# Performance work log

Hardware: AMD Instinct MI355X
Metric: run time of the kernel (lower is better)

## Reference

```python
import jax, jax.numpy as jnp
import numpy as np

EMBED = 1024
HEADS = 16
HDIM = 64
FF = 4 * EMBED
EPS = 1e-5


def layer_norm(x, g, b):
    mu = jnp.mean(x, axis=-1, keepdims=True)
    var = jnp.var(x, axis=-1, keepdims=True)
    return (x - mu) * jax.lax.rsqrt(var + EPS) * g + b


def setup_inputs() -> dict:
    key = jax.random.key(0)
    ks = jax.random.split(key, 12)
    s = lambda fan_in: 1.0 / np.sqrt(fan_in)
    return {
        "x": jax.random.normal(ks[0], (2, 2048, EMBED), jnp.float32),
        "w_qkv": jax.random.uniform(ks[1], (EMBED, 3 * HEADS * HDIM), jnp.float32, -s(EMBED), s(EMBED)),
        "w_proj": jax.random.uniform(ks[2], (HEADS * HDIM, EMBED), jnp.float32, -s(HEADS * HDIM), s(HEADS * HDIM)),
        "b_proj": jax.random.uniform(ks[3], (EMBED,), jnp.float32, -s(HEADS * HDIM), s(HEADS * HDIM)),
        "w1": jax.random.uniform(ks[4], (EMBED, FF), jnp.float32, -s(EMBED), s(EMBED)),
        "b1": jax.random.uniform(ks[5], (FF,), jnp.float32, -s(EMBED), s(EMBED)),
        "w2": jax.random.uniform(ks[6], (FF, EMBED), jnp.float32, -s(FF), s(FF)),
        "b2": jax.random.uniform(ks[7], (EMBED,), jnp.float32, -s(FF), s(FF)),
        "g1": jnp.ones((EMBED,), jnp.float32),
        "be1": jnp.zeros((EMBED,), jnp.float32),
        "g2": jnp.ones((EMBED,), jnp.float32),
        "be2": jnp.zeros((EMBED,), jnp.float32),
    }


def reference(x, w_qkv, w_proj, b_proj, w1, b1, w2, b2, g1, be1, g2, be2):
    bs, seq, _ = x.shape
    # --- MHA on pre-norm ---
    h = layer_norm(x, g1, be1)
    qkv = h @ w_qkv  # [b, s, 3*H*D]
    qkv = qkv.reshape(bs, seq, HEADS, 3, HDIM)
    q = qkv[:, :, :, 0, :]  # [b, s, h, d]
    k = qkv[:, :, :, 1, :]
    v = qkv[:, :, :, 2, :]
    attn = jnp.einsum("bqhd,bkhd->bhqk", q, k) / np.sqrt(HDIM)
    causal = jnp.tril(jnp.ones((seq, seq), bool))
    attn = jnp.where(causal, attn, -jnp.inf)
    attn = jax.nn.softmax(attn, axis=-1)
    out = jnp.einsum("bhqk,bkhd->bhqd", attn, v)
    # Faithful to original bug: .view without transposing heads back.
    out = out.reshape(bs, seq, HEADS * HDIM)
    out = out @ w_proj + b_proj
    x = x + out
    # --- FFN on pre-norm ---
    h2 = layer_norm(x, g2, be2)
    ff = jax.nn.relu(h2 @ w1 + b1) @ w2 + b2
    return x + ff
```

## Files before the change

### kernel.cpp

```cpp
#include <hip/hip_runtime.h>
#include <cstdint>

#define EMBED 1024
#define HEADS 16
#define HDIM  64
#define SEQ   2048
#define BATCH 2
#define ROWS  (BATCH*SEQ)

typedef __bf16 bf16x8 __attribute__((ext_vector_type(8)));
typedef float  f32x4  __attribute__((ext_vector_type(4)));
typedef float  f32x16 __attribute__((ext_vector_type(16)));
typedef unsigned int uint32x2 __attribute__((ext_vector_type(2)));

__device__ __forceinline__ unsigned short f2bf(float f) {
    union { float f; uint32_t u; } v; v.f = f;
    uint32_t r = v.u + 0x7fffu + ((v.u >> 16) & 1u);
    return (unsigned short)(r >> 16);
}

__device__ __forceinline__ uint32_t cvtpk_bf16(float lo, float hi) {
    uint32_t r;
    asm("v_cvt_pk_bf16_f32 %0, %1, %2" : "=v"(r) : "v"(lo), "v"(hi));
    return r;
}

__device__ __forceinline__ float fexp2(float x) {
    float r;
    asm("v_exp_f32 %0, %1" : "=v"(r) : "v"(x));
    return r;
}

#define GLDS(src, dst) __builtin_amdgcn_global_load_lds( \
    (const __attribute__((address_space(1))) uint32_t*)(src), \
    (__attribute__((address_space(3))) uint32_t*)(dst), 16, 0, 0)

__global__ __launch_bounds__(256) void k_transpose_all(
    const float* __restrict__ w_qkv, const float* __restrict__ w_proj,
    const float* __restrict__ w1,    const float* __restrict__ w2,
    unsigned short* __restrict__ wqkvT, unsigned short* __restrict__ wprojT,
    unsigned short* __restrict__ w1T,   unsigned short* __restrict__ w2T)
{
    int b = blockIdx.x;
    const float* in; unsigned short* out; int N, K, nx;
    if (b < 3072)      {           in = w_qkv;  out = wqkvT;  K = 1024; N = 3072; nx = 96; }
    else if (b < 4096) { b -= 3072; in = w_proj; out = wprojT; K = 1024; N = 1024; nx = 32; }
    else if (b < 8192) { b -= 4096; in = w1;     out = w1T;    K = 1024; N = 4096; nx = 128; }
    else               { b -= 8192; in = w2;     out = w2T;    K = 4096; N = 1024; nx = 32; }
    const int n0 = (b % nx) * 32, k0 = (b / nx) * 32;

    __shared__ float tile[32][33];
    const int tx = threadIdx.x & 31, ty = threadIdx.x >> 5;
#pragma unroll
    for (int r = 0; r < 4; ++r)
        tile[ty + 8*r][tx] = in[(size_t)(k0 + ty + 8*r) * N + n0 + tx];
    __syncthreads();
#pragma unroll
    for (int r = 0; r < 4; ++r)
        out[(size_t)(n0 + ty + 8*r) * K + k0 + tx] = f2bf(tile[tx][ty + 8*r]);
}

__global__ __launch_bounds__(256) void k_layernorm(
    const float* __restrict__ x, const float* __restrict__ g, const float* __restrict__ b,
    unsigned short* __restrict__ h)
{
    const int row = blockIdx.x, t = threadIdx.x;
    float4 v = ((const float4*)(x + (size_t)row * EMBED))[t];
    float s = v.x + v.y + v.z + v.w;
    float q = v.x*v.x + v.y*v.y + v.z*v.z + v.w*v.w;
#pragma unroll
    for (int off = 32; off >= 1; off >>= 1) {
        s += __shfl_xor(s, off, 64);
        q += __shfl_xor(q, off, 64);
    }
    __shared__ float ss[4], sq[4];
    if ((t & 63) == 0) { ss[t >> 6] = s; sq[t >> 6] = q; }
    __syncthreads();
    s = ss[0] + ss[1] + ss[2] + ss[3];
    q = sq[0] + sq[1] + sq[2] + sq[3];
    const float mu  = s * (1.0f / EMBED);
    const float var = q * (1.0f / EMBED) - mu * mu;
    const float rs  = rsqrtf(var + 1e-5f);
    float4 gv = ((const float4*)g)[t];
    float4 bv = ((const float4*)b)[t];
    ushort4 o;
    o.x = f2bf((v.x - mu) * rs * gv.x + bv.x);
    o.y = f2bf((v.y - mu) * rs * gv.y + bv.y);
    o.z = f2bf((v.z - mu) * rs * gv.z + bv.z);
    o.w = f2bf((v.w - mu) * rs * gv.w + bv.w);
    ((ushort4*)(h + (size_t)row * EMBED))[t] = o;
}

template<int FLAGS, typename OutT>
__global__ __launch_bounds__(512) void k_gemm_bt(
    const unsigned short* __restrict__ A,
    const unsigned short* __restrict__ BT,
    const float* __restrict__ bias,
    const float* __restrict__ resid,
    OutT* __restrict__ C,
    int M, int N, int K)
{
    __shared__ uint4 ldsv[8192];
    char* base = (char*)ldsv;
    char* aL = base;
    char* bL = base + 16384;
    const int t = threadIdx.x, l = t & 63, w = t >> 6;
    const int pos = w & 3, kh = w >> 2;
    const int qr = pos >> 1, qc = pos & 1;
    const int g = l >> 4, c = l & 15;

    const int gx = gridDim.x;
    const int lin = blockIdx.y * gx + blockIdx.x;
    const int cpx = (gx * gridDim.y) >> 3;
    const int swz = (lin & 7) * cpx + (lin >> 3);
    const int row0 = (swz / gx) * 128, col0 = (swz % gx) * 128;

    const int swc = (((l & 7) ^ (l >> 3)) * 8);
    const int rA0 = w*16 + (l >> 3), rA1 = rA0 + 8;
    const unsigned short* aS0 = A  + (size_t)(row0 + rA0) * K + swc;
    const unsigned short* aS1 = A  + (size_t)(row0 + rA1) * K + swc;
    const unsigned short* bS0 = BT + (size_t)(col0 + rA0) * K + swc;
    const unsigned short* bS1 = BT + (size_t)(col0 + rA1) * K + swc;
    const int dst0 = w * 2048, dst1 = w * 2048 + 1024;

    f32x4 acc[4][4];
#pragma unroll
    for (int m = 0; m < 4; ++m)
#pragma unroll
        for (int n = 0; n < 4; ++n) acc[m][n] = f32x4{0.f, 0.f, 0.f, 0.f};

    auto stage = [&](int kt, int bo) {
        const size_t ko = (size_t)kt * 64;
        GLDS(aS0 + ko, aL + bo + dst0);
        GLDS(aS1 + ko, aL + bo + dst1);
        GLDS(bS0 + ko, bL + bo + dst0);
        GLDS(bS1 + ko, bL + bo + dst1);
    };
    auto compute = [&](int bo) {
        const int chb = ((kh*4 + g) ^ (c & 7)) * 16;
        bf16x8 af[4], bfr[4];
#pragma unroll
        for (int m = 0; m < 4; ++m)
            af[m] = *(const bf16x8*)(aL + bo + (qr*64 + m*16 + c) * 128 + chb);
#pragma unroll
        for (int n = 0; n < 4; ++n)
            bfr[n] = *(const bf16x8*)(bL + bo + (qc*64 + n*16 + c) * 128 + chb);
        __builtin_amdgcn_s_setprio(1);
#pragma unroll
        for (int m = 0; m < 4; ++m)
#pragma unroll
            for (int n = 0; n < 4; ++n)
                acc[m][n] = __builtin_amdgcn_mfma_f32_16x16x32_bf16(af[m], bfr[n], acc[m][n], 0, 0, 0);
        __builtin_amdgcn_s_setprio(0);
    };

    const int nkt = K >> 6;
    stage(0, 0);
    stage(1, 32768);
    for (int kt = 0; kt < nkt; ++kt) {
        const int bo = (kt & 3) * 32768;
        if (kt + 2 < nkt) {
            stage(kt + 2, ((kt + 2) & 3) * 32768);
            asm volatile("s_waitcnt vmcnt(8)" ::: "memory");
        } else if (kt + 1 < nkt) {
            asm volatile("s_waitcnt vmcnt(4)" ::: "memory");
        } else {
            asm volatile("s_waitcnt vmcnt(0)" ::: "memory");
        }
        __builtin_amdgcn_s_barrier();
        compute(bo);
    }

    asm volatile("s_waitcnt lgkmcnt(0)" ::: "memory");
    __builtin_amdgcn_s_barrier();
    if (kh) {
#pragma unroll
        for (int m = 0; m < 4; ++m)
#pragma unroll
            for (int n = 0; n < 4; ++n)
                *(f32x4*)(base + (((pos*16 + m*4 + n) * 64) + l) * 16) = acc[m][n];
    }
    asm volatile("s_waitcnt lgkmcnt(0)" ::: "memory");
    __builtin_amdgcn_s_barrier();

    if (!kh) {
#pragma unroll
        for (int m = 0; m < 4; ++m) {
            const int rb = row0 + qr*64 + m*16 + g*4;
#pragma unroll
            for (int n = 0; n < 4; ++n) {
                const f32x4 part = *(const f32x4*)(base + (((pos*16 + m*4 + n) * 64) + l) * 16);
                const int col = col0 + qc*64 + n*16 + c;
                float bv = 0.f;
                if constexpr ((FLAGS & 1) != 0) bv = bias[col];
#pragma unroll
                for (int j = 0; j < 4; ++j) {
                    float v = acc[m][n][j] + part[j] + bv;
                    if constexpr ((FLAGS & 2) != 0) v = fmaxf(v, 0.f);
                    if constexpr ((FLAGS & 4) != 0) v += resid[(size_t)(rb + j) * N + col];
                    if constexpr (sizeof(OutT) == 2) C[(size_t)(rb + j) * N + col] = (OutT)f2bf(v);
                    else                             C[(size_t)(rb + j) * N + col] = v;
                }
            }
        }
    }
}

template<int FLAGS, typename OutT>
__global__ __launch_bounds__(512) __attribute__((amdgpu_waves_per_eu(2, 2)))
void k_gemm256(
    const unsigned short* __restrict__ A,
    const unsigned short* __restrict__ BT,
    const float* __restrict__ bias,
    OutT* __restrict__ C,
    unsigned short* __restrict__ Qo,
    unsigned short* __restrict__ Ko,
    unsigned short* __restrict__ Vo,
    int M, int N, int K)
{
    __shared__ uint4 ldsv[8192];
    char* base = (char*)ldsv;
    const int t = threadIdx.x, l = t & 63, w = t >> 6;
    const int wr = w >> 2, wc = w & 3;
    const int g = l >> 4, c = l & 15;

    const int gx = gridDim.x;
    const int lin = blockIdx.y * gx + blockIdx.x;
    const int cpx = (gx * gridDim.y) >> 3;
    const int swz = (lin & 7) * cpx + (lin >> 3);
    const int row0 = (swz / gx) * 256, col0 = (swz % gx) * 256;

    const int srow = l >> 2;
    const int sch  = (l & 3) ^ ((l >> 3) & 3);
    const unsigned short* aS0 = A  + (size_t)(row0 + w*32 +      srow) * K + sch*8;
    const unsigned short* aS1 = A  + (size_t)(row0 + w*32 + 16 + srow) * K + sch*8;
    const unsigned short* bS0 = BT + (size_t)(col0 + w*32 +      srow) * K + sch*8;
    const unsigned short* bS1 = BT + (size_t)(col0 + w*32 + 16 + srow) * K + sch*8;
    const int dA0 = w*2048, dA1 = w*2048 + 1024;

    f32x4 acc[8][4];
#pragma unroll
    for (int m = 0; m < 8; ++m)
#pragma unroll
        for (int n = 0; n < 4; ++n) acc[m][n] = f32x4{0.f, 0.f, 0.f, 0.f};

    auto stage = [&](int kt, int bo) {
        const size_t ko = (size_t)kt * 32;
        GLDS(aS0 + ko, base + bo + dA0);
        GLDS(aS1 + ko, base + bo + dA1);
        GLDS(bS0 + ko, base + bo + 16384 + dA0);
        GLDS(bS1 + ko, base + bo + 16384 + dA1);
    };
    auto compute = [&](int bo) {
        const int chb = (g ^ ((c >> 1) & 3)) * 16;
        bf16x8 af[8], bfr[4];
#pragma unroll
        for (int m = 0; m < 8; ++m)
            af[m] = *(const bf16x8*)(base + bo + (wr*128 + m*16 + c) * 64 + chb);
#pragma unroll
        for (int n = 0; n < 4; ++n)
            bfr[n] = *(const bf16x8*)(base + bo + 16384 + (wc*64 + n*16 + c) * 64 + chb);
        __builtin_amdgcn_s_setprio(1);
#pragma unroll
        for (int m = 0; m < 8; ++m)
#pragma unroll
            for (int n = 0; n < 4; ++n)
                acc[m][n] = __builtin_amdgcn_mfma_f32_16x16x32_bf16(af[m], bfr[n], acc[m][n], 0, 0, 0);
        __builtin_amdgcn_s_setprio(0);
    };

    const int nkt = K >> 5;
    stage(0, 0);
    stage(1, 32768);
    for (int kt = 0; kt < nkt; ++kt) {
        const int bo = (kt & 3) * 32768;
        if (kt + 2 < nkt) {
            stage(kt + 2, ((kt + 2) & 3) * 32768);
            asm volatile("s_waitcnt vmcnt(8)" ::: "memory");
        } else if (kt + 1 < nkt) {
            asm volatile("s_waitcnt vmcnt(4)" ::: "memory");
        } else {
            asm volatile("s_waitcnt vmcnt(0)" ::: "memory");
        }
        __builtin_amdgcn_s_barrier();
        compute(bo);
    }

    if constexpr ((FLAGS & 8) != 0) {
#pragma unroll
        for (int m = 0; m < 8; ++m) {
            const int rb = row0 + wr*128 + m*16 + g*4;
            const int b  = rb >> 11;
            const int q0 = rb & 2047;
#pragma unroll
            for (int n = 0; n < 4; ++n) {
                const int col = col0 + wc*64 + n*16 + c;
                const int hh  = col / 192;
                const int rem = col - hh * 192;
                const int tt  = rem >> 6;
                const int d   = rem & 63;
                const int bhh = b * HEADS + hh;
                if (tt == 2) {
                    const int st_e = q0 >> 6, kk = q0 & 63;
                    const int f_e  = (d >> 5) * 4 + (kk >> 4);
                    const int ln_e = ((kk >> 3) & 1) * 32 + (d & 31);
                    const int e0   = kk & 7;
                    ushort4 o;
                    o.x = f2bf(acc[m][n][0]); o.y = f2bf(acc[m][n][1]);
                    o.z = f2bf(acc[m][n][2]); o.w = f2bf(acc[m][n][3]);
                    *(ushort4*)(Vo + (size_t)bhh * (SEQ*HDIM) + st_e*4096 + f_e*512 + ln_e*8 + e0) = o;
                } else if (tt == 1) {
                    const int st_e = q0 >> 6;
                    const int f_e  = ((q0 >> 5) & 1) * 4 + (d >> 4);
                    const int lq_e = q0 & 31;
                    const int ln_b = ((d >> 3) & 1) * 32;
                    const int e_e  = d & 7;
                    unsigned short* dst = Ko + (size_t)bhh * (SEQ*HDIM) + st_e*4096 + f_e*512
                                             + (ln_b + lq_e)*8 + e_e;
#pragma unroll
                    for (int j = 0; j < 4; ++j)
                        dst[j*8] = f2bf(acc[m][n][j]);
                } else {
                    unsigned short* dst = Qo + ((size_t)bhh * SEQ + q0) * HDIM + d;
#pragma unroll
                    for (int j = 0; j < 4; ++j)
                        dst[(size_t)j * HDIM] = f2bf(acc[m][n][j]);
                }
            }
        }
    } else {
#pragma unroll
        for (int m = 0; m < 8; ++m) {
            const int rb = row0 + wr*128 + m*16 + g*4;
#pragma unroll
            for (int n = 0; n < 4; ++n) {
                const int col = col0 + wc*64 + n*16 + c;
                float bv = 0.f;
                if constexpr ((FLAGS & 1) != 0) bv = bias[col];
#pragma unroll
                for (int j = 0; j < 4; ++j) {
                    float v = acc[m][n][j] + bv;
                    if constexpr ((FLAGS & 2) != 0) v = fmaxf(v, 0.f);
                    if constexpr (sizeof(OutT) == 2) C[(size_t)(rb + j) * N + col] = (OutT)f2bf(v);
                    else                             C[(size_t)(rb + j) * N + col] = v;
                }
            }
        }
    }
}

__global__ __launch_bounds__(512) __attribute__((amdgpu_waves_per_eu(2, 2)))
void k_attention(
    const unsigned short* __restrict__ Qb,
    const unsigned short* __restrict__ Kf,
    const unsigned short* __restrict__ Vf,
    unsigned short* __restrict__ out)
{
    const int t = threadIdx.x, l = t & 63, w = t >> 6;
    const int lq = l & 31, hi = l >> 5;
    const int bid = blockIdx.x;
    const int sbid = (bid & 7) * 32 + (bid >> 3);
    const int bh = sbid >> 3, j = sbid & 7;
    const int qb = (w < 4) ? (4*j + w) : (63 - 4*j - (w - 4));
    const int q  = qb * 32 + lq;

    const unsigned short* Qh  = Qb + (size_t)bh * SEQ * HDIM;
    const unsigned short* Kfh = Kf + (size_t)bh * SEQ * HDIM + l*8;
    const unsigned short* Vfh = Vf + (size_t)bh * SEQ * HDIM + l*8;

    const bf16x8 qf0 = *(const bf16x8*)(Qh + (size_t)q * HDIM      + hi*8);
    const bf16x8 qf1 = *(const bf16x8*)(Qh + (size_t)q * HDIM + 16 + hi*8);
    const bf16x8 qf2 = *(const bf16x8*)(Qh + (size_t)q * HDIM + 32 + hi*8);
    const bf16x8 qf3 = *(const bf16x8*)(Qh + (size_t)q * HDIM + 48 + hi*8);

    f32x16 oT0, oT1;
#pragma unroll
    for (int i = 0; i < 16; ++i) { oT0[i] = 0.f; oT1[i] = 0.f; }
    float lacc0 = 0.f, lacc1 = 0.f, lacc2 = 0.f, lacc3 = 0.f;
    const float kSc = 0.18033688011112042f;
    const int nst = (qb >> 1) + 1;

    bf16x8 kA0, kA1, kA2, kA3, kA4, kA5, kA6, kA7;
    bf16x8 kB0, kB1, kB2, kB3, kB4, kB5, kB6, kB7;

#define LOADK(stv, KF) do {                                                     \
    const unsigned short* kp_ = Kfh + (size_t)(stv) * 4096;                     \
    KF##0 = *(const bf16x8*)(kp_ +    0); KF##1 = *(const bf16x8*)(kp_ +  512); \
    KF##2 = *(const bf16x8*)(kp_ + 1024); KF##3 = *(const bf16x8*)(kp_ + 1536); \
    KF##4 = *(const bf16x8*)(kp_ + 2048); KF##5 = *(const bf16x8*)(kp_ + 2560); \
    KF##6 = *(const bf16x8*)(kp_ + 3072); KF##7 = *(const bf16x8*)(kp_ + 3584); \
} while (0)

#define STEP(stv, KF) do {                                                      \
    const int kv0_ = (stv) * 64;                                                \
    const unsigned short* vp_ = Vfh + (size_t)(stv) * 4096;                     \
    bf16x8 vf0_ = *(const bf16x8*)(vp_ +    0), vf1_ = *(const bf16x8*)(vp_ +  512); \
    bf16x8 vf2_ = *(const bf16x8*)(vp_ + 1024), vf3_ = *(const bf16x8*)(vp_ + 1536); \
    bf16x8 vf4_ = *(const bf16x8*)(vp_ + 2048), vf5_ = *(const bf16x8*)(vp_ + 2560); \
    bf16x8 vf6_ = *(const bf16x8*)(vp_ + 3072), vf7_ = *(const bf16x8*)(vp_ + 3584); \
    f32x16 sA_, sB_;                                                            \
    _Pragma("unroll")                                                           \
    for (int i = 0; i < 16; ++i) { sA_[i] = 0.f; sB_[i] = 0.f; }               \
    __builtin_amdgcn_s_setprio(1);                                              \
    sA_ = __builtin_amdgcn_mfma_f32_32x32x16_bf16(KF##0, qf0, sA_, 0, 0, 0);    \
    sA_ = __builtin_amdgcn_mfma_f32_32x32x16_bf16(KF##1, qf1, sA_, 0, 0, 0);    \
    sA_ = __builtin_amdgcn_mfma_f32_32x32x16_bf16(KF##2, qf2, sA_, 0, 0, 0);    \
    sA_ = __builtin_amdgcn_mfma_f32_32x32x16_bf16(KF##3, qf3, sA_, 0, 0, 0);    \
    sB_ = __builtin_amdgcn_mfma_f32_32x32x16_bf16(KF##4, qf0, sB_, 0, 0, 0);    \
    sB_ = __builtin_amdgcn_mfma_f32_32x32x16_bf16(KF##5, qf1, sB_, 0, 0, 0);    \
    sB_ = __builtin_amdgcn_mfma_f32_32x32x16_bf16(KF##6, qf2, sB_, 0, 0, 0);    \
    sB_ = __builtin_amdgcn_mfma_f32_32x32x16_bf16(KF##7, qf3, sB_, 0, 0, 0);    \
    __builtin_amdgcn_s_setprio(0);                                              \
    float p_[32];                                                               \
    if ((stv) == nst - 1) {                                                     \
        _Pragma("unroll")                                                       \
        for (int r = 0; r < 16; ++r) {                                          \
            const int key_ = kv0_ + (r & 3) + 8*(r >> 2) + 4*hi;                \
            p_[r]      = (key_      <= q) ? fexp2(sA_[r] * kSc) : 0.f;          \
            p_[16 + r] = (key_ + 32 <= q) ? fexp2(sB_[r] * kSc) : 0.f;          \
        }                                                                       \
    } else {                                                                    \
        _Pragma("unroll")                                                       \
        for (int r = 0; r < 16; ++r) {                                          \
            p_[r]      = fexp2(sA_[r] * kSc);                                   \
            p_[16 + r] = fexp2(sB_[r] * kSc);                                   \
        }                                                                       \
    }                                                                           \
    _Pragma("unroll")                                                           \
    for (int i = 0; i < 32; i += 4) {                                           \
        lacc0 += p_[i]; lacc1 += p_[i+1]; lacc2 += p_[i+2]; lacc3 += p_[i+3];   \
    }                                                                           \
    bf16x8 pa_[4];                                                              \
    _Pragma("unroll")                                                           \
    for (int ks = 0; ks < 4; ++ks) {                                            \
        const int b8_ = ks * 8;                                                 \
        uint32x2 rA_ = __builtin_amdgcn_permlane32_swap(                        \
            cvtpk_bf16(p_[b8_+0], p_[b8_+1]), cvtpk_bf16(p_[b8_+4], p_[b8_+5]), false, false); \
        uint32x2 rB_ = __builtin_amdgcn_permlane32_swap(                        \
            cvtpk_bf16(p_[b8_+2], p_[b8_+3]), cvtpk_bf16(p_[b8_+6], p_[b8_+7]), false, false); \
        union { uint32_t u[4]; bf16x8 v; } pk_;                                 \
        pk_.u[0] = rA_[0]; pk_.u[1] = rB_[0]; pk_.u[2] = rA_[1]; pk_.u[3] = rB_[1]; \
        pa_[ks] = pk_.v;                                                        \
    }                                                                           \
    __builtin_amdgcn_s_setprio(1);                                              \
    oT0 = __builtin_amdgcn_mfma_f32_32x32x16_bf16(vf0_, pa_[0], oT0, 0, 0, 0);  \
    oT0 = __builtin_amdgcn_mfma_f32_32x32x16_bf16(vf1_, pa_[1], oT0, 0, 0, 0);  \
    oT0 = __builtin_amdgcn_mfma_f32_32x32x16_bf16(vf2_, pa_[2], oT0, 0, 0, 0);  \
    oT0 = __builtin_amdgcn_mfma_f32_32x32x16_bf16(vf3_, pa_[3], oT0, 0, 0, 0);  \
    oT1 = __builtin_amdgcn_mfma_f32_32x32x16_bf16(vf4_, pa_[0], oT1, 0, 0, 0);  \
    oT1 = __builtin_amdgcn_mfma_f32_32x32x16_bf16(vf5_, pa_[1], oT1, 0, 0, 0);  \
    oT1 = __builtin_amdgcn_mfma_f32_32x32x16_bf16(vf6_, pa_[2], oT1, 0, 0, 0);  \
    oT1 = __builtin_amdgcn_mfma_f32_32x32x16_bf16(vf7_, pa_[3], oT1, 0, 0, 0);  \
    __builtin_amdgcn_s_setprio(0);                                              \
} while (0)

    LOADK(0, kA);
    int st = 0;
    for (;;) {
        if (st + 1 < nst) LOADK(st + 1, kB);
        STEP(st, kA);
        if (++st >= nst) break;
        if (st + 1 < nst) LOADK(st + 1, kA);
        STEP(st, kB);
        if (++st >= nst) break;
    }
#undef LOADK
#undef STEP

    float lsum = (lacc0 + lacc1) + (lacc2 + lacc3);
    lsum += __shfl_xor(lsum, 32, 64);
    const float inv = 1.f / lsum;
    unsigned short* ob = out + ((size_t)bh * SEQ + q) * HDIM;
#pragma unroll
    for (int m2 = 0; m2 < 4; ++m2) {
        ushort4 o0, o1;
        o0.x = f2bf(oT0[m2*4+0] * inv); o0.y = f2bf(oT0[m2*4+1] * inv);
        o0.z = f2bf(oT0[m2*4+2] * inv); o0.w = f2bf(oT0[m2*4+3] * inv);
        o1.x = f2bf(oT1[m2*4+0] * inv); o1.y = f2bf(oT1[m2*4+1] * inv);
        o1.z = f2bf(oT1[m2*4+2] * inv); o1.w = f2bf(oT1[m2*4+3] * inv);
        *(ushort4*)(ob +      m2*8 + hi*4) = o0;
        *(ushort4*)(ob + 32 + m2*8 + hi*4) = o1;
    }
}

extern "C" void kernel_launch(void* const* d_in, const int* in_sizes, int n_in,
                              void* d_out, int out_size, void* d_ws, size_t ws_size,
                              hipStream_t stream)
{
    (void)in_sizes; (void)n_in; (void)out_size; (void)ws_size;
    const float* x      = (const float*)d_in[0];
    const float* w_qkv  = (const float*)d_in[1];
    const float* w_proj = (const float*)d_in[2];
    const float* b_proj = (const float*)d_in[3];
    const float* w1     = (const float*)d_in[4];
    const float* b1     = (const float*)d_in[5];
    const float* w2     = (const float*)d_in[6];
    const float* b2     = (const float*)d_in[7];
    const float* g1     = (const float*)d_in[8];
    const float* be1    = (const float*)d_in[9];
    const float* g2     = (const float*)d_in[10];
    const float* be2    = (const float*)d_in[11];

    char* ws = (char*)d_ws;
    size_t o = 0;
    auto take = [&](size_t bytes) -> char* {
        char* p = ws + o;
        o += (bytes + 255) & ~(size_t)255;
        return p;
    };
    unsigned short* wqkvT  = (unsigned short*)take(3072ull * 1024 * 2);
    unsigned short* wprojT = (unsigned short*)take(1024ull * 1024 * 2);
    unsigned short* w1T    = (unsigned short*)take(4096ull * 1024 * 2);
    unsigned short* w2T    = (unsigned short*)take(1024ull * 4096 * 2);
    unsigned short* h      = (unsigned short*)take(4096ull * 1024 * 2);
    unsigned short* Qb     = (unsigned short*)take(4096ull * 1024 * 2);
    unsigned short* Kfb    = (unsigned short*)take(4096ull * 1024 * 2);
    unsigned short* Vfb    = (unsigned short*)take(4096ull * 1024 * 2);
    unsigned short* attno  = (unsigned short*)take(4096ull * 1024 * 2);
    float*          x2     = (float*)take(4096ull * 1024 * 4);
    unsigned short* f1     = Qb;

    k_transpose_all<<<12288, 256, 0, stream>>>(
        w_qkv, w_proj, w1, w2, wqkvT, wprojT, w1T, w2T);

    k_layernorm<<<4096, 256, 0, stream>>>(x, g1, be1, h);
    k_gemm256<8, unsigned short><<<dim3(12, 16), 512, 0, stream>>>(
        h, wqkvT, nullptr, (unsigned short*)nullptr, Qb, Kfb, Vfb, ROWS, 3072, 1024);
    k_attention<<<256, 512, 0, stream>>>(Qb, Kfb, Vfb, attno);
    k_gemm_bt<5, float><<<dim3(8, 32), 512, 0, stream>>>(
        attno, wprojT, b_proj, x, x2, ROWS, 1024, 1024);
    k_layernorm<<<4096, 256, 0, stream>>>(x2, g2, be2, h);
    k_gemm256<3, unsigned short><<<dim3(16, 16), 512, 0, stream>>>(
        h, w1T, b1, f1, nullptr, nullptr, nullptr, ROWS, 4096, 1024);
    k_gemm_bt<5, float><<<dim3(8, 32), 512, 0, stream>>>(
        f1, w2T, b2, x2, (float*)d_out, ROWS, 1024, 4096);
}
```

Measured before the change: 181.4 us.

## Add dedicated QKV GEMM with 256x192 tiles and fuse first layernorm into prep

Replaces the generic 256x256 GEMM for the QKV projection with a dedicated kernel that uses 256x192 tiles. The 16x16 grid gives 256 blocks instead of 192, and each tile's columns line up with one head's Q/K/V group. The new kernel uses a 64-wide K step, double-buffered LDS with an XOR swizzle, and setprio around the MFMA bursts. The first layernorm is folded into the weight-transpose launch as extra blocks, removing one kernel launch. The trade-offs are a shallower prefetch pipeline than the original 4-stage one, and a one-pass variance formula (E[x²]−mean²) that may lose some precision.

After: 176.4 us, median of 2. 1.03x faster.

```diff
diff --git a/kernel.cpp b/kernel.cpp
--- a/kernel.cpp
+++ b/kernel.cpp
@@ -35,13 +35,43 @@
     (const __attribute__((address_space(1))) uint32_t*)(src), \
     (__attribute__((address_space(3))) uint32_t*)(dst), 16, 0, 0)
 
-__global__ __launch_bounds__(256) void k_transpose_all(
+__global__ __launch_bounds__(256) void k_prep(
     const float* __restrict__ w_qkv, const float* __restrict__ w_proj,
     const float* __restrict__ w1,    const float* __restrict__ w2,
     unsigned short* __restrict__ wqkvT, unsigned short* __restrict__ wprojT,
-    unsigned short* __restrict__ w1T,   unsigned short* __restrict__ w2T)
+    unsigned short* __restrict__ w1T,   unsigned short* __restrict__ w2T,
+    const float* __restrict__ x, const float* __restrict__ g1,
+    const float* __restrict__ be1, unsigned short* __restrict__ h)
 {
     int b = blockIdx.x;
+    if (b >= 12288) {
+        const int row = b - 12288, t = threadIdx.x;
+        float4 v = ((const float4*)(x + (size_t)row * EMBED))[t];
+        float s = v.x + v.y + v.z + v.w;
+        float q = v.x*v.x + v.y*v.y + v.z*v.z + v.w*v.w;
+#pragma unroll
+        for (int off = 32; off >= 1; off >>= 1) {
+            s += __shfl_xor(s, off, 64);
+            q += __shfl_xor(q, off, 64);
+        }
+        __shared__ float ss[4], sq[4];
+        if ((t & 63) == 0) { ss[t >> 6] = s; sq[t >> 6] = q; }
+        __syncthreads();
+        s = ss[0] + ss[1] + ss[2] + ss[3];
+        q = sq[0] + sq[1] + sq[2] + sq[3];
+        const float mu  = s * (1.0f / EMBED);
+        const float var = q * (1.0f / EMBED) - mu * mu;
+        const float rs  = rsqrtf(var + 1e-5f);
+        float4 gv = ((const float4*)g1)[t];
+        float4 bv = ((const float4*)be1)[t];
+        ushort4 o;
+        o.x = f2bf((v.x - mu) * rs * gv.x + bv.x);
+        o.y = f2bf((v.y - mu) * rs * gv.y + bv.y);
+        o.z = f2bf((v.z - mu) * rs * gv.z + bv.z);
+        o.w = f2bf((v.w - mu) * rs * gv.w + bv.w);
+        ((ushort4*)(h + (size_t)row * EMBED))[t] = o;
+        return;
+    }
     const float* in; unsigned short* out; int N, K, nx;
     if (b < 3072)      {           in = w_qkv;  out = wqkvT;  K = 1024; N = 3072; nx = 96; }
     else if (b < 4096) { b -= 3072; in = w_proj; out = wprojT; K = 1024; N = 1024; nx = 32; }
@@ -213,9 +243,6 @@
     const unsigned short* __restrict__ BT,
     const float* __restrict__ bias,
     OutT* __restrict__ C,
-    unsigned short* __restrict__ Qo,
-    unsigned short* __restrict__ Ko,
-    unsigned short* __restrict__ Vo,
     int M, int N, int K)
 {
     __shared__ uint4 ldsv[8192];
@@ -286,64 +313,150 @@
         compute(bo);
     }
 
-    if constexpr ((FLAGS & 8) != 0) {
-#pragma unroll
-        for (int m = 0; m < 8; ++m) {
-            const int rb = row0 + wr*128 + m*16 + g*4;
-            const int b  = rb >> 11;
-            const int q0 = rb & 2047;
-#pragma unroll
-            for (int n = 0; n < 4; ++n) {
-                const int col = col0 + wc*64 + n*16 + c;
-                const int hh  = col / 192;
-                const int rem = col - hh * 192;
-                const int tt  = rem >> 6;
-                const int d   = rem & 63;
-                const int bhh = b * HEADS + hh;
-                if (tt == 2) {
-                    const int st_e = q0 >> 6, kk = q0 & 63;
-                    const int f_e  = (d >> 5) * 4 + (kk >> 4);
-                    const int ln_e = ((kk >> 3) & 1) * 32 + (d & 31);
-                    const int e0   = kk & 7;
-                    ushort4 o;
-                    o.x = f2bf(acc[m][n][0]); o.y = f2bf(acc[m][n][1]);
-                    o.z = f2bf(acc[m][n][2]); o.w = f2bf(acc[m][n][3]);
-                    *(ushort4*)(Vo + (size_t)bhh * (SEQ*HDIM) + st_e*4096 + f_e*512 + ln_e*8 + e0) = o;
-                } else if (tt == 1) {
-                    const int st_e = q0 >> 6;
-                    const int f_e  = ((q0 >> 5) & 1) * 4 + (d >> 4);
-                    const int lq_e = q0 & 31;
-                    const int ln_b = ((d >> 3) & 1) * 32;
-                    const int e_e  = d & 7;
-                    unsigned short* dst = Ko + (size_t)bhh * (SEQ*HDIM) + st_e*4096 + f_e*512
-                                             + (ln_b + lq_e)*8 + e_e;
-#pragma unroll
-                    for (int j = 0; j < 4; ++j)
-                        dst[j*8] = f2bf(acc[m][n][j]);
-                } else {
-                    unsigned short* dst = Qo + ((size_t)bhh * SEQ + q0) * HDIM + d;
-#pragma unroll
-                    for (int j = 0; j < 4; ++j)
-                        dst[(size_t)j * HDIM] = f2bf(acc[m][n][j]);
+#pragma unroll
+    for (int m = 0; m < 8; ++m) {
+        const int rb = row0 + wr*128 + m*16 + g*4;
+#pragma unroll
+        for (int n = 0; n < 4; ++n) {
+            const int col = col0 + wc*64 + n*16 + c;
+            float bv = 0.f;
+            if constexpr ((FLAGS & 1) != 0) bv = bias[col];
+#pragma unroll
+            for (int j = 0; j < 4; ++j) {
+                float v = acc[m][n][j] + bv;
+                if constexpr ((FLAGS & 2) != 0) v = fmaxf(v, 0.f);
+                if constexpr (sizeof(OutT) == 2) C[(size_t)(rb + j) * N + col] = (OutT)f2bf(v);
+                else                             C[(size_t)(rb + j) * N + col] = v;
+            }
+        }
+    }
+}
+
+__global__ __launch_bounds__(512) __attribute__((amdgpu_waves_per_eu(2, 2)))
+void k_gemm_qkv(
+    const unsigned short* __restrict__ A,
+    const unsigned short* __restrict__ BT,
+    unsigned short* __restrict__ Qo,
+    unsigned short* __restrict__ Ko,
+    unsigned short* __restrict__ Vo,
+    int K)
+{
+    __shared__ uint4 ldsv[8192];
+    char* base = (char*)ldsv;
+    const int t = threadIdx.x, l = t & 63, w = t >> 6;
+    const int wr = w >> 2, wc = w & 3;
+    const int g = l >> 4, c = l & 15;
+
+    const int gx = gridDim.x;
+    const int lin = blockIdx.y * gx + blockIdx.x;
+    const int cpx = (gx * gridDim.y) >> 3;
+    const int swz = (lin & 7) * cpx + (lin >> 3);
+    const int row0 = (swz / gx) * 256, col0 = (swz % gx) * 192;
+
+    const int sr = l >> 3, sc = l & 7;
+    const int swk = (sc ^ sr) * 8;
+    const unsigned short* aSr = A  + (size_t)(row0 + w*32 + sr) * K + swk;
+    const unsigned short* bSr = BT + (size_t)(col0 + w*24 + sr) * K + swk;
+
+    f32x4 acc[8][3];
+#pragma unroll
+    for (int m = 0; m < 8; ++m)
+#pragma unroll
+        for (int n = 0; n < 3; ++n) acc[m][n] = f32x4{0.f, 0.f, 0.f, 0.f};
+
+    auto stage = [&](int kt, int bo) {
+        const size_t ko = (size_t)kt * 64;
+#pragma unroll
+        for (int i = 0; i < 4; ++i)
+            GLDS(aSr + ko + (size_t)(i*8) * K, base + bo + w*4096 + i*1024);
+#pragma unroll
+        for (int i = 0; i < 3; ++i)
+            GLDS(bSr + ko + (size_t)(i*8) * K, base + bo + 32768 + w*3072 + i*1024);
+    };
+
+    const int nkt = K >> 6;
+    stage(0, 0);
+    asm volatile("s_waitcnt vmcnt(0)" ::: "memory");
+    __builtin_amdgcn_s_barrier();
+    int bufo = 0;
+    for (int kt = 0; kt < nkt; ++kt) {
+        if (kt + 1 < nkt) stage(kt + 1, bufo ^ 65536);
+        bf16x8 bfr[3][2];
+#pragma unroll
+        for (int n = 0; n < 3; ++n)
+#pragma unroll
+            for (int ks = 0; ks < 2; ++ks) {
+                const int r = wc*48 + n*16 + c;
+                bfr[n][ks] = *(const bf16x8*)(base + bufo + 32768 + r*128
+                                              + (((ks*4 + g) ^ (c & 7)) * 16));
+            }
+#pragma unroll
+        for (int p = 0; p < 4; ++p) {
+            bf16x8 af[2][2];
+#pragma unroll
+            for (int mi = 0; mi < 2; ++mi)
+#pragma unroll
+                for (int ks = 0; ks < 2; ++ks) {
+                    const int r = wr*128 + (p*2 + mi)*16 + c;
+                    af[mi][ks] = *(const bf16x8*)(base + bufo + r*128
+                                                  + (((ks*4 + g) ^ (c & 7)) * 16));
                 }
-            }
-        }
-    } else {
-#pragma unroll
-        for (int m = 0; m < 8; ++m) {
-            const int rb = row0 + wr*128 + m*16 + g*4;
-#pragma unroll
-            for (int n = 0; n < 4; ++n) {
-                const int col = col0 + wc*64 + n*16 + c;
-                float bv = 0.f;
-                if constexpr ((FLAGS & 1) != 0) bv = bias[col];
-#pragma unroll
-                for (int j = 0; j < 4; ++j) {
-                    float v = acc[m][n][j] + bv;
-                    if constexpr ((FLAGS & 2) != 0) v = fmaxf(v, 0.f);
-                    if constexpr (sizeof(OutT) == 2) C[(size_t)(rb + j) * N + col] = (OutT)f2bf(v);
-                    else                             C[(size_t)(rb + j) * N + col] = v;
-                }
+            __builtin_amdgcn_s_setprio(1);
+#pragma unroll
+            for (int ks = 0; ks < 2; ++ks)
+#pragma unroll
+                for (int mi = 0; mi < 2; ++mi)
+#pragma unroll
+                    for (int n = 0; n < 3; ++n)
+                        acc[p*2 + mi][n] = __builtin_amdgcn_mfma_f32_16x16x32_bf16(
+                            af[mi][ks], bfr[n][ks], acc[p*2 + mi][n], 0, 0, 0);
+            __builtin_amdgcn_s_setprio(0);
+        }
+        if (kt + 1 < nkt) {
+            asm volatile("s_waitcnt vmcnt(0)" ::: "memory");
+            __builtin_amdgcn_s_barrier();
+            bufo ^= 65536;
+        }
+    }
+
+#pragma unroll
+    for (int m = 0; m < 8; ++m) {
+        const int rb = row0 + wr*128 + m*16 + g*4;
+        const int b  = rb >> 11;
+        const int q0 = rb & 2047;
+#pragma unroll
+        for (int n = 0; n < 3; ++n) {
+            const int col = col0 + wc*48 + n*16 + c;
+            const int hh  = col / 192;
+            const int rem = col - hh * 192;
+            const int tt  = rem >> 6;
+            const int d   = rem & 63;
+            const int bhh = b * HEADS + hh;
+            if (tt == 2) {
+                const int st_e = q0 >> 6, kk = q0 & 63;
+                const int f_e  = (d >> 5) * 4 + (kk >> 4);
+                const int ln_e = ((kk >> 3) & 1) * 32 + (d & 31);
+                const int e0   = kk & 7;
+                ushort4 o;
+                o.x = f2bf(acc[m][n][0]); o.y = f2bf(acc[m][n][1]);
+                o.z = f2bf(acc[m][n][2]); o.w = f2bf(acc[m][n][3]);
+                *(ushort4*)(Vo + (size_t)bhh * (SEQ*HDIM) + st_e*4096 + f_e*512 + ln_e*8 + e0) = o;
+            } else if (tt == 1) {
+                const int st_e = q0 >> 6;
+                const int f_e  = ((q0 >> 5) & 1) * 4 + (d >> 4);
+                const int lq_e = q0 & 31;
+                const int ln_b = ((d >> 3) & 1) * 32;
+                const int e_e  = d & 7;
+                unsigned short* dst = Ko + (size_t)bhh * (SEQ*HDIM) + st_e*4096 + f_e*512
+                                         + (ln_b + lq_e)*8 + e_e;
+#pragma unroll
+                for (int j = 0; j < 4; ++j)
+                    dst[j*8] = f2bf(acc[m][n][j]);
+            } else {
+                unsigned short* dst = Qo + ((size_t)bhh * SEQ + q0) * HDIM + d;
+#pragma unroll
+                for (int j = 0; j < 4; ++j)
+                    dst[(size_t)j * HDIM] = f2bf(acc[m][n][j]);
             }
         }
     }
@@ -520,18 +633,16 @@
     float*          x2     = (float*)take(4096ull * 1024 * 4);
     unsigned short* f1     = Qb;
 
-    k_transpose_all<<<12288, 256, 0, stream>>>(
-        w_qkv, w_proj, w1, w2, wqkvT, wprojT, w1T, w2T);
-
-    k_layernorm<<<4096, 256, 0, stream>>>(x, g1, be1, h);
-    k_gemm256<8, unsigned short><<<dim3(12, 16), 512, 0, stream>>>(
-        h, wqkvT, nullptr, (unsigned short*)nullptr, Qb, Kfb, Vfb, ROWS, 3072, 1024);
+    k_prep<<<16384, 256, 0, stream>>>(
+        w_qkv, w_proj, w1, w2, wqkvT, wprojT, w1T, w2T, x, g1, be1, h);
+
+    k_gemm_qkv<<<dim3(16, 16), 512, 0, stream>>>(h, wqkvT, Qb, Kfb, Vfb, 1024);
     k_attention<<<256, 512, 0, stream>>>(Qb, Kfb, Vfb, attno);
     k_gemm_bt<5, float><<<dim3(8, 32), 512, 0, stream>>>(
         attno, wprojT, b_proj, x, x2, ROWS, 1024, 1024);
     k_layernorm<<<4096, 256, 0, stream>>>(x2, g2, be2, h);
     k_gemm256<3, unsigned short><<<dim3(16, 16), 512, 0, stream>>>(
-        h, w1T, b1, f1, nullptr, nullptr, nullptr, ROWS, 4096, 1024);
+        h, w1T, b1, f1, ROWS, 4096, 1024);
     k_gemm_bt<5, float><<<dim3(8, 32), 512, 0, stream>>>(
         f1, w2T, b2, x2, (float*)d_out, ROWS, 1024, 4096);
 }
```
